# Performance work log

Measured on AMD Instinct MI355X. Metric: run time of the kernel, lower is better.

Reference implementation:

```python
import jax, jax.numpy as jnp
import numpy as np

B, INPUT_DIM, OUTPUT_DIM, Z_DIM = 32, 2048, 2048, 64
NNZ = 209715


def setup_inputs() -> dict:
    key = jax.random.key(0)
    k_x, k_z, k_w, k_b = jax.random.split(key, 4)
    x = jax.random.normal(k_x, (B, INPUT_DIM), dtype=jnp.float32)
    z = jax.random.normal(k_z, (B, Z_DIM), dtype=jnp.float32)
    W_net = jax.random.normal(k_w, (Z_DIM, NNZ), dtype=jnp.float32) * 0.02
    b_net = jax.random.normal(k_b, (NNZ,), dtype=jnp.float32) * 0.02
    # unique nonzero positions of output_matrix [INPUT_DIM, OUTPUT_DIM]
    rng = np.random.default_rng(0)
    lin = rng.choice(INPUT_DIM * OUTPUT_DIM, size=NNZ, replace=False)
    in_idx = jnp.asarray(lin // OUTPUT_DIM, dtype=jnp.int32)   # rows  -> input dim
    out_idx = jnp.asarray(lin % OUTPUT_DIM, dtype=jnp.int32)   # cols  -> output dim
    return {"x": x, "z": z, "W_net": W_net, "b_net": b_net,
            "in_idx": in_idx, "out_idx": out_idx}


def reference(x, z, W_net, b_net, in_idx, out_idx):
    # hypernetwork: net(z) -> [B, NNZ] matrix entries
    mat_entity = z @ W_net + b_net                      # [B, NNZ]
    # scatter into zero-filled dense matrix: mat[:, out_idx, in_idx] = entries
    mat = jnp.zeros((x.shape[0], OUTPUT_DIM, INPUT_DIM), dtype=x.dtype)
    mat = mat.at[:, out_idx, in_idx].set(mat_entity)    # [B, O, I]
    # batched matvec
    return jnp.einsum('boi,bi->bo', mat, x)             # [B, O]
```

## Files before the change

kernel.cpp:

```cpp
#include <hip/hip_runtime.h>
#include <hip/hip_bf16.h>

#define BATCH   32
#define IN_DIM  2048
#define OUT_DIM 2048
#define ZDIM    64
#define NNZ     209715
#define CAP     160
#define TILES   ((NNZ + 15) / 16)
#define TPW     2
#define CWAVES  ((TILES + TPW - 1) / TPW)
#define CBLOCKS ((CWAVES + 3) / 4)
#define NBLK    ((NNZ + 1023) / 1024)

typedef __attribute__((ext_vector_type(8))) short bf16x8;
typedef __attribute__((ext_vector_type(4))) float f32x4;

#define OFF_XT    0
#define OFF_ZBF   262144
#define OFF_CNT   266240
#define OFF_BH    274432
#define OFF_COMBO 2371584
#define OFF_E     3210496
#define B_WS_NEEDED (OFF_E + (size_t)OUT_DIM * CAP * BATCH * 2)

__device__ __forceinline__ short f2bf(float f) {
    unsigned u = __float_as_uint(f);
    u += 0x7fffu + ((u >> 16) & 1u);
    return (short)(u >> 16);
}

__global__ __launch_bounds__(1024) void hist_prep(
    const int* __restrict__ out_idx, const float* __restrict__ x,
    const float* __restrict__ z, int* __restrict__ bh,
    int* __restrict__ combo, float* __restrict__ xT, short* __restrict__ zbf)
{
    __shared__ int lh[OUT_DIM];
    const int t = threadIdx.x, blk = blockIdx.x;
    lh[t] = 0; lh[t + 1024] = 0;
    __syncthreads();
    const int gid = blk * 1024 + t;
    if (gid < BATCH * IN_DIM) {
        const int b = gid >> 11, i = gid & 2047;
        xT[i * BATCH + b] = x[gid];
        if (gid < BATCH * ZDIM) zbf[gid] = f2bf(z[gid]);
    }
    if (gid < NNZ) {
        const int oi = out_idx[gid];
        const int r  = atomicAdd(&lh[oi], 1);
        combo[gid] = (r << 11) | oi;
    }
    __syncthreads();
    bh[t * 256 + blk]          = lh[t];
    bh[(t + 1024) * 256 + blk] = lh[t + 1024];
}

__global__ __launch_bounds__(256) void colscan(
    int* __restrict__ bh, int* __restrict__ cnt)
{
    const int o    = blockIdx.x * 4 + (threadIdx.x >> 6);
    const int lane = threadIdx.x & 63;
    const int i0   = lane * 4;
    int4 v = *reinterpret_cast<int4*>(bh + o * 256 + i0);
    const int a = (i0 + 0 < NBLK) ? v.x : 0;
    const int b = (i0 + 1 < NBLK) ? v.y : 0;
    const int c = (i0 + 2 < NBLK) ? v.z : 0;
    const int d = (i0 + 3 < NBLK) ? v.w : 0;
    const int s1 = a + b, s2 = s1 + c, tot = s2 + d;
    int inc = tot;
    #pragma unroll
    for (int t = 1; t < 64; t <<= 1) {
        const int n = __shfl_up(inc, t);
        if (lane >= t) inc += n;
    }
    const int exc = inc - tot;
    int4 w; w.x = exc; w.y = exc + a; w.z = exc + s1; w.w = exc + s2;
    *reinterpret_cast<int4*>(bh + o * 256 + i0) = w;
    if (lane == 63) cnt[o] = inc;
}

__global__ __launch_bounds__(256, 4) void compute_mfma(
    const short* __restrict__ zbf, const float* __restrict__ W,
    const float* __restrict__ bn, const int* __restrict__ in_idx,
    const int* __restrict__ combo, const int* __restrict__ bh,
    const float* __restrict__ xT, short* __restrict__ E)
{
    const int lane = threadIdx.x & 63;
    const int m    = lane & 15;
    const int hi   = lane >> 4;
    const int wid  = blockIdx.x * 4 + (threadIdx.x >> 6);
    const int t0   = wid * TPW;
    if (t0 >= TILES) return;

    bf16x8 zf[2][2];
    #pragma unroll
    for (int bt = 0; bt < 2; ++bt)
        #pragma unroll
        for (int jt = 0; jt < 2; ++jt)
            zf[bt][jt] = *reinterpret_cast<const bf16x8*>(
                zbf + (bt * 16 + m) * ZDIM + jt * 32 + hi * 8);

    int rowL[2] = {-1, -1}, iiL[2] = {0, 0};
    float bnL[2] = {0.f, 0.f};
    #pragma unroll
    for (int tt = 0; tt < TPW; ++tt) {
        const int t = t0 + tt;
        if (t < TILES && lane < 16) {
            const int kk = t * 16 + lane;
            if (kk < NNZ) {
                iiL[tt] = in_idx[kk];
                bnL[tt] = bn[kk];
                const int cb  = combo[kk];
                const int oi  = cb & 2047;
                const int pos = bh[oi * 256 + (kk >> 10)] + (cb >> 11);
                rowL[tt] = (pos < CAP) ? oi * CAP + pos : -1;
            }
        }
    }

    float wv[2][16];
    #pragma unroll
    for (int tt = 0; tt < TPW; ++tt) {
        const int t  = (t0 + tt < TILES) ? (t0 + tt) : (TILES - 1);
        const int kA = (t * 16 + m < NNZ) ? (t * 16 + m) : (NNZ - 1);
        const float* wp = W + (size_t)(hi * 8) * NNZ + kA;
        #pragma unroll
        for (int e = 0; e < 8; ++e) wv[tt][e]     = wp[(size_t)e * NNZ];
        #pragma unroll
        for (int e = 0; e < 8; ++e) wv[tt][8 + e] = wp[(size_t)(32 + e) * NNZ];
    }

    float x0_[2][4], x1_[2][4];
    #pragma unroll
    for (int tt = 0; tt < TPW; ++tt)
        #pragma unroll
        for (int r = 0; r < 4; ++r) {
            const int ii = __shfl(iiL[tt], hi * 4 + r);
            x0_[tt][r] = xT[ii * BATCH + m];
            x1_[tt][r] = xT[ii * BATCH + 16 + m];
        }

    #pragma unroll
    for (int tt = 0; tt < TPW; ++tt) {
        union { bf16x8 v; short s[8]; } a0, a1;
        #pragma unroll
        for (int e = 0; e < 8; ++e) { a0.s[e] = f2bf(wv[tt][e]); a1.s[e] = f2bf(wv[tt][8 + e]); }

        f32x4 acc0 = {0.f, 0.f, 0.f, 0.f};
        f32x4 acc1 = {0.f, 0.f, 0.f, 0.f};
        acc0 = __builtin_amdgcn_mfma_f32_16x16x32_bf16(a0.v, zf[0][0], acc0, 0, 0, 0);
        acc0 = __builtin_amdgcn_mfma_f32_16x16x32_bf16(a1.v, zf[0][1], acc0, 0, 0, 0);
        acc1 = __builtin_amdgcn_mfma_f32_16x16x32_bf16(a0.v, zf[1][0], acc1, 0, 0, 0);
        acc1 = __builtin_amdgcn_mfma_f32_16x16x32_bf16(a1.v, zf[1][1], acc1, 0, 0, 0);

        #pragma unroll
        for (int r = 0; r < 4; ++r) {
            const int src = hi * 4 + r;
            const int row = __shfl(rowL[tt], src);
            if (row >= 0) {
                const float bb = __shfl(bnL[tt], src);
                short* Ep = E + (size_t)row * BATCH;
                Ep[m]      = f2bf((acc0[r] + bb) * x0_[tt][r]);
                Ep[16 + m] = f2bf((acc1[r] + bb) * x1_[tt][r]);
            }
        }
    }
}

__global__ __launch_bounds__(256) void reduce_bf16(
    const short* __restrict__ E, const int* __restrict__ cnt,
    float* __restrict__ out)
{
    const int o    = blockIdx.x * 4 + (threadIdx.x >> 6);
    const int lane = threadIdx.x & 63;
    const int r  = lane >> 2;
    const int bg = lane & 3;
    const int s = o * CAP;
    int c = cnt[o]; if (c > CAP) c = CAP;
    const int e = s + c;

    float acc[8];
    #pragma unroll
    for (int q = 0; q < 8; ++q) acc[q] = 0.f;

    for (int p = s + r; p < e; p += 16) {
        const uint4 v = *reinterpret_cast<const uint4*>(E + (size_t)p * BATCH + bg * 8);
        const unsigned u[4] = {v.x, v.y, v.z, v.w};
        #pragma unroll
        for (int q = 0; q < 4; ++q) {
            acc[2 * q]     += __uint_as_float((u[q] & 0xFFFFu) << 16);
            acc[2 * q + 1] += __uint_as_float(u[q] & 0xFFFF0000u);
        }
    }

    #pragma unroll
    for (int d = 4; d < 64; d <<= 1)
        #pragma unroll
        for (int q = 0; q < 8; ++q)
            acc[q] += __shfl_xor(acc[q], d);

    if (lane < 4) {
        #pragma unroll
        for (int q = 0; q < 8; ++q)
            out[(bg * 8 + q) * OUT_DIM + o] = acc[q];
    }
}

__global__ __launch_bounds__(256) void hyper_scatter_kernel(
    const float* __restrict__ x, const float* __restrict__ z,
    const float* __restrict__ W, const float* __restrict__ bn,
    const int* __restrict__ in_idx, const int* __restrict__ out_idx,
    float* __restrict__ out)
{
    __shared__ float zs[BATCH * ZDIM];
    const int tid = threadIdx.x;
    {
        const float4* zg  = reinterpret_cast<const float4*>(z);
        float4*       zsv = reinterpret_cast<float4*>(zs);
        zsv[tid]       = zg[tid];
        zsv[tid + 256] = zg[tid + 256];
    }
    __syncthreads();
    const int k = blockIdx.x * 256 + tid;
    if (k >= NNZ) return;
    float w[ZDIM];
    #pragma unroll
    for (int j = 0; j < ZDIM; ++j) w[j] = W[(size_t)j * NNZ + k];
    const float bk = bn[k];
    const int ii = in_idx[k], oi = out_idx[k];
    const float4* zv = reinterpret_cast<const float4*>(zs);
    #pragma unroll
    for (int b = 0; b < BATCH; ++b) {
        float e = bk;
        #pragma unroll
        for (int j4 = 0; j4 < ZDIM / 4; ++j4) {
            const float4 zz = zv[b * (ZDIM / 4) + j4];
            e = fmaf(zz.x, w[j4 * 4 + 0], e);
            e = fmaf(zz.y, w[j4 * 4 + 1], e);
            e = fmaf(zz.z, w[j4 * 4 + 2], e);
            e = fmaf(zz.w, w[j4 * 4 + 3], e);
        }
        atomicAdd(&out[b * OUT_DIM + oi], e * x[b * IN_DIM + ii]);
    }
}

extern "C" void kernel_launch(void* const* d_in, const int* in_sizes, int n_in,
                              void* d_out, int out_size, void* d_ws, size_t ws_size,
                              hipStream_t stream) {
    const float* x       = (const float*)d_in[0];
    const float* z       = (const float*)d_in[1];
    const float* W       = (const float*)d_in[2];
    const float* bn      = (const float*)d_in[3];
    const int*   in_idx  = (const int*)d_in[4];
    const int*   out_idx = (const int*)d_in[5];
    float*       out     = (float*)d_out;
    char*        ws      = (char*)d_ws;

    if (ws_size >= B_WS_NEEDED) {
        float* xT    = (float*)(ws + OFF_XT);
        short* zbf   = (short*)(ws + OFF_ZBF);
        int*   cnt   = (int*)(ws + OFF_CNT);
        int*   bh    = (int*)(ws + OFF_BH);
        int*   combo = (int*)(ws + OFF_COMBO);
        short* E     = (short*)(ws + OFF_E);

        hist_prep<<<NBLK, 1024, 0, stream>>>(out_idx, x, z, bh, combo, xT, zbf);
        colscan  <<<OUT_DIM / 4, 256, 0, stream>>>(bh, cnt);
        compute_mfma<<<CBLOCKS, 256, 0, stream>>>(zbf, W, bn, in_idx, combo, bh, xT, E);
        reduce_bf16 <<<OUT_DIM / 4, 256, 0, stream>>>(E, cnt, out);
    } else {
        hipMemsetAsync(out, 0, (size_t)BATCH * OUT_DIM * sizeof(float), stream);
        const int grid = (NNZ + 255) / 256;
        hyper_scatter_kernel<<<grid, 256, 0, stream>>>(x, z, W, bn, in_idx, out_idx, out);
    }
}
```

Baseline: 41.23 us.

## Replace per-block histogram plus column scan with global atomic slot allocation

Drops the separate colscan kernel. Each hist_prep block now reserves its slot ranges directly through atomicAdd on a global per-column counter (zeroed by a memset) and writes the final row index per nonzero, so compute_mfma reads one precomputed row instead of combo plus bh. Slot order within a column becomes nondeterministic, which changes the summation order only. Also adds sched barriers to group the loads in compute_mfma, and splits each output column's reduction across two waves that are combined through shared memory.

```diff
diff --git a/kernel.cpp b/kernel.cpp
--- a/kernel.cpp
+++ b/kernel.cpp
@@ -19,9 +19,8 @@
 #define OFF_XT    0
 #define OFF_ZBF   262144
 #define OFF_CNT   266240
-#define OFF_BH    274432
-#define OFF_COMBO 2371584
-#define OFF_E     3210496
+#define OFF_ROW   274432
+#define OFF_E     1113600
 #define B_WS_NEEDED (OFF_E + (size_t)OUT_DIM * CAP * BATCH * 2)
 
 __device__ __forceinline__ short f2bf(float f) {
@@ -32,10 +31,11 @@
 
 __global__ __launch_bounds__(1024) void hist_prep(
     const int* __restrict__ out_idx, const float* __restrict__ x,
-    const float* __restrict__ z, int* __restrict__ bh,
-    int* __restrict__ combo, float* __restrict__ xT, short* __restrict__ zbf)
+    const float* __restrict__ z, int* __restrict__ cnt,
+    int* __restrict__ rowOf, float* __restrict__ xT, short* __restrict__ zbf)
 {
     __shared__ int lh[OUT_DIM];
+    __shared__ int base[OUT_DIM];
     const int t = threadIdx.x, blk = blockIdx.x;
     lh[t] = 0; lh[t + 1024] = 0;
     __syncthreads();
@@ -45,45 +45,30 @@
         xT[i * BATCH + b] = x[gid];
         if (gid < BATCH * ZDIM) zbf[gid] = f2bf(z[gid]);
     }
+    int oi = -1, r = 0;
     if (gid < NNZ) {
-        const int oi = out_idx[gid];
-        const int r  = atomicAdd(&lh[oi], 1);
-        combo[gid] = (r << 11) | oi;
-    }
-    __syncthreads();
-    bh[t * 256 + blk]          = lh[t];
-    bh[(t + 1024) * 256 + blk] = lh[t + 1024];
-}
-
-__global__ __launch_bounds__(256) void colscan(
-    int* __restrict__ bh, int* __restrict__ cnt)
-{
-    const int o    = blockIdx.x * 4 + (threadIdx.x >> 6);
-    const int lane = threadIdx.x & 63;
-    const int i0   = lane * 4;
-    int4 v = *reinterpret_cast<int4*>(bh + o * 256 + i0);
-    const int a = (i0 + 0 < NBLK) ? v.x : 0;
-    const int b = (i0 + 1 < NBLK) ? v.y : 0;
-    const int c = (i0 + 2 < NBLK) ? v.z : 0;
-    const int d = (i0 + 3 < NBLK) ? v.w : 0;
-    const int s1 = a + b, s2 = s1 + c, tot = s2 + d;
-    int inc = tot;
-    #pragma unroll
-    for (int t = 1; t < 64; t <<= 1) {
-        const int n = __shfl_up(inc, t);
-        if (lane >= t) inc += n;
-    }
-    const int exc = inc - tot;
-    int4 w; w.x = exc; w.y = exc + a; w.z = exc + s1; w.w = exc + s2;
-    *reinterpret_cast<int4*>(bh + o * 256 + i0) = w;
-    if (lane == 63) cnt[o] = inc;
+        oi = out_idx[gid];
+        r  = atomicAdd(&lh[oi], 1);
+    }
+    __syncthreads();
+    {
+        const int c0 = lh[t];
+        base[t] = c0 ? atomicAdd(&cnt[t], c0) : 0;
+        const int c1 = lh[t + 1024];
+        base[t + 1024] = c1 ? atomicAdd(&cnt[t + 1024], c1) : 0;
+    }
+    __syncthreads();
+    if (oi >= 0) {
+        const int pos = base[oi] + r;
+        rowOf[gid] = (pos < CAP) ? oi * CAP + pos : -1;
+    }
 }
 
 __global__ __launch_bounds__(256, 4) void compute_mfma(
     const short* __restrict__ zbf, const float* __restrict__ W,
     const float* __restrict__ bn, const int* __restrict__ in_idx,
-    const int* __restrict__ combo, const int* __restrict__ bh,
-    const float* __restrict__ xT, short* __restrict__ E)
+    const int* __restrict__ rowOf, const float* __restrict__ xT,
+    short* __restrict__ E)
 {
     const int lane = threadIdx.x & 63;
     const int m    = lane & 15;
@@ -92,14 +77,6 @@
     const int t0   = wid * TPW;
     if (t0 >= TILES) return;
 
-    bf16x8 zf[2][2];
-    #pragma unroll
-    for (int bt = 0; bt < 2; ++bt)
-        #pragma unroll
-        for (int jt = 0; jt < 2; ++jt)
-            zf[bt][jt] = *reinterpret_cast<const bf16x8*>(
-                zbf + (bt * 16 + m) * ZDIM + jt * 32 + hi * 8);
-
     int rowL[2] = {-1, -1}, iiL[2] = {0, 0};
     float bnL[2] = {0.f, 0.f};
     #pragma unroll
@@ -108,15 +85,20 @@
         if (t < TILES && lane < 16) {
             const int kk = t * 16 + lane;
             if (kk < NNZ) {
-                iiL[tt] = in_idx[kk];
-                bnL[tt] = bn[kk];
-                const int cb  = combo[kk];
-                const int oi  = cb & 2047;
-                const int pos = bh[oi * 256 + (kk >> 10)] + (cb >> 11);
-                rowL[tt] = (pos < CAP) ? oi * CAP + pos : -1;
+                rowL[tt] = rowOf[kk];
+                iiL[tt]  = in_idx[kk];
+                bnL[tt]  = bn[kk];
             }
         }
     }
+
+    bf16x8 zf[2][2];
+    #pragma unroll
+    for (int bt = 0; bt < 2; ++bt)
+        #pragma unroll
+        for (int jt = 0; jt < 2; ++jt)
+            zf[bt][jt] = *reinterpret_cast<const bf16x8*>(
+                zbf + (bt * 16 + m) * ZDIM + jt * 32 + hi * 8);
 
     float wv[2][16];
     #pragma unroll
@@ -129,6 +111,7 @@
         #pragma unroll
         for (int e = 0; e < 8; ++e) wv[tt][8 + e] = wp[(size_t)(32 + e) * NNZ];
     }
+    __builtin_amdgcn_sched_barrier(0);
 
     float x0_[2][4], x1_[2][4];
     #pragma unroll
@@ -139,6 +122,7 @@
             x0_[tt][r] = xT[ii * BATCH + m];
             x1_[tt][r] = xT[ii * BATCH + 16 + m];
         }
+    __builtin_amdgcn_sched_barrier(0);
 
     #pragma unroll
     for (int tt = 0; tt < TPW; ++tt) {
@@ -171,8 +155,12 @@
     const short* __restrict__ E, const int* __restrict__ cnt,
     float* __restrict__ out)
 {
-    const int o    = blockIdx.x * 4 + (threadIdx.x >> 6);
+    __shared__ float partial[2][BATCH];
+    const int wave = threadIdx.x >> 6;
     const int lane = threadIdx.x & 63;
+    const int cs   = wave >> 1;
+    const int part = wave & 1;
+    const int o    = blockIdx.x * 2 + cs;
     const int r  = lane >> 2;
     const int bg = lane & 3;
     const int s = o * CAP;
@@ -183,7 +171,7 @@
     #pragma unroll
     for (int q = 0; q < 8; ++q) acc[q] = 0.f;
 
-    for (int p = s + r; p < e; p += 16) {
+    for (int p = s + part * 16 + r; p < e; p += 32) {
         const uint4 v = *reinterpret_cast<const uint4*>(E + (size_t)p * BATCH + bg * 8);
         const unsigned u[4] = {v.x, v.y, v.z, v.w};
         #pragma unroll
@@ -199,10 +187,15 @@
         for (int q = 0; q < 8; ++q)
             acc[q] += __shfl_xor(acc[q], d);
 
-    if (lane < 4) {
+    if (part == 1 && lane < 4) {
+        #pragma unroll
+        for (int q = 0; q < 8; ++q) partial[cs][bg * 8 + q] = acc[q];
+    }
+    __syncthreads();
+    if (part == 0 && lane < 4) {
         #pragma unroll
         for (int q = 0; q < 8; ++q)
-            out[(bg * 8 + q) * OUT_DIM + o] = acc[q];
+            out[(bg * 8 + q) * OUT_DIM + o] = acc[q] + partial[cs][bg * 8 + q];
     }
 }
 
@@ -260,14 +253,13 @@
         float* xT    = (float*)(ws + OFF_XT);
         short* zbf   = (short*)(ws + OFF_ZBF);
         int*   cnt   = (int*)(ws + OFF_CNT);
-        int*   bh    = (int*)(ws + OFF_BH);
-        int*   combo = (int*)(ws + OFF_COMBO);
+        int*   rowOf = (int*)(ws + OFF_ROW);
         short* E     = (short*)(ws + OFF_E);
 
-        hist_prep<<<NBLK, 1024, 0, stream>>>(out_idx, x, z, bh, combo, xT, zbf);
-        colscan  <<<OUT_DIM / 4, 256, 0, stream>>>(bh, cnt);
-        compute_mfma<<<CBLOCKS, 256, 0, stream>>>(zbf, W, bn, in_idx, combo, bh, xT, E);
-        reduce_bf16 <<<OUT_DIM / 4, 256, 0, stream>>>(E, cnt, out);
+        hipMemsetAsync(cnt, 0, OUT_DIM * sizeof(int), stream);
+        hist_prep<<<NBLK, 1024, 0, stream>>>(out_idx, x, z, cnt, rowOf, xT, zbf);
+        compute_mfma<<<CBLOCKS, 256, 0, stream>>>(zbf, W, bn, in_idx, rowOf, xT, E);
+        reduce_bf16 <<<OUT_DIM / 2, 256, 0, stream>>>(E, cnt, out);
     } else {
         hipMemsetAsync(out, 0, (size_t)BATCH * OUT_DIM * sizeof(float), stream);
         const int grid = (NNZ + 255) / 256;
```

Result: faster. 40.38 us (-2.1%).
